# Optimization experiments

Measured on AMD Instinct MI355X. Metric: run time of the kernel, lower is better.

The kernel has to match this reference:

```python
import jax, jax.numpy as jnp
import numpy as np

B, SEQ, NVAR, DM, K = 2, 512, 64, 128, 2
SCALE = DM ** -0.5  # ScaledDotProductAttention scale, lsa=False so constant


def _period_branch(x4, Wel, bel, Wq, bq, Wk, bk, Wv, bv, Wo, bo, period):
    # x4: [B, DM(time), NVAR, DM(dim)] -- output of start_embed
    pad = (-DM) % period
    pn = (DM + pad) // period  # period_num
    xp = jnp.pad(x4, ((0, 0), (0, pad), (0, 0), (0, 0)))
    # torch .unfold(dim=1, size=period, step=period) -> [B, pn, NVAR, DM, period]
    xw = xp.reshape(B, pn, period, NVAR, DM).transpose(0, 1, 3, 4, 2)
    # emb_linear over the d_model (dim) axis
    xw = jnp.einsum('bqndl,ed->bqnel', xw, Wel) + bel[None, None, None, :, None]
    # -> [B, NVAR, dim, pn, period] then flatten to conv1d layout [bn, dim, L]
    X = xw.transpose(0, 2, 3, 1, 4).reshape(B * NVAR, DM, pn * period)
    # 1x1 Conv1d QKV projections over the channel (dim) axis
    q = jnp.einsum('bdl,ed->bel', X, Wq) + bq[None, :, None]
    k = jnp.einsum('bdl,ed->bel', X, Wk) + bk[None, :, None]
    v = jnp.einsum('bdl,ed->bel', X, Wv) + bv[None, :, None]
    q_s = q.reshape(B * NVAR, DM, pn, period).transpose(0, 1, 3, 2)  # [bn,dim,pl,pn]
    k_s = k.reshape(B * NVAR, DM, pn, period)                         # [bn,dim,pn,pl]
    v_s = v.reshape(B * NVAR, DM, pn, period).transpose(0, 1, 3, 2)  # [bn,dim,pl,pn]
    attn = jax.nn.softmax(jnp.einsum('bdip,bdpj->bdij', q_s, k_s) * SCALE, axis=-1)
    o = jnp.einsum('bdij,bdjp->bdip', attn, v_s)  # [bn, dim, period, pn]
    o = o.reshape(B * NVAR, DM, period * pn)[:, :, :DM]  # truncate to n_heads=DM
    return o @ Wo.T + bo  # to_out Linear(n_heads, n_heads), dropout eval-mode


def reference(x, W_emb, b_emb, W_start, b_start, Wel, bel, Wq, bq, Wk, bk, Wv, bv, Wo, bo, f1, f2):
    # inverted embedding: Linear(seq_len->d_model) over time, then permute -> [B, DM, NVAR]
    xe = (jnp.einsum('bsn,sd->bnd', x, W_emb) + b_emb).transpose(0, 2, 1)
    # FFT_for_Period amplitudes; top-k frequency indices f1,f2 are static (host-side in torch)
    amp = jnp.abs(jnp.fft.rfft(xe, axis=1)).mean(-1)  # [B, DM//2+1]
    pw = jax.nn.softmax(jnp.stack([amp[:, f1], amp[:, f2]], -1), axis=-1)  # [B, K]
    # start_embed: Linear(1 -> d_model) -> [B, DM, NVAR, DM]
    x4 = xe[..., None] * W_start + b_start
    outs = [_period_branch(x4, Wel, bel, Wq, bq, Wk, bk, Wv, bv, Wo, bo, DM // f)
            for f in (f1, f2)]
    res = jnp.stack(outs, -1)                      # [B*NVAR, DM, DM, K]
    pw_b = jnp.repeat(pw, NVAR, axis=0)            # [B*NVAR, K] (b-major order matches reshape)
    out = (res * pw_b[:, None, None, :]).sum(-1)
    return out.reshape(B, NVAR, DM, DM)


def setup_inputs() -> dict:
    key = jax.random.key(0)
    ks = jax.random.split(key, 16)
    s = 0.02
    d = {
        'x': jax.random.normal(ks[0], (B, SEQ, NVAR), jnp.float32),
        'W_emb': jax.random.normal(ks[1], (SEQ, DM), jnp.float32) * s,
        'b_emb': jax.random.normal(ks[2], (DM,), jnp.float32) * s,
        'W_start': jax.random.normal(ks[3], (DM,), jnp.float32) * s,
        'b_start': jax.random.normal(ks[4], (DM,), jnp.float32) * s,
        'Wel': jax.random.normal(ks[5], (DM, DM), jnp.float32) * s,
        'bel': jax.random.normal(ks[6], (DM,), jnp.float32) * s,
        'Wq': jax.random.normal(ks[7], (DM, DM), jnp.float32) * s,
        'bq': jax.random.normal(ks[8], (DM,), jnp.float32) * s,
        'Wk': jax.random.normal(ks[9], (DM, DM), jnp.float32) * s,
        'bk': jax.random.normal(ks[10], (DM,), jnp.float32) * s,
        'Wv': jax.random.normal(ks[11], (DM, DM), jnp.float32) * s,
        'bv': jax.random.normal(ks[12], (DM,), jnp.float32) * s,
        'Wo': jax.random.normal(ks[13], (DM, DM), jnp.float32) * s,
        'bo': jax.random.normal(ks[14], (DM,), jnp.float32) * s,
    }
    # host-side FFT period detection, mirroring torch's .detach().cpu().numpy() topk
    xe = np.einsum('bsn,sd->bnd', np.asarray(d['x']), np.asarray(d['W_emb'])) + np.asarray(d['b_emb'])
    xe = xe.transpose(0, 2, 1)  # [B, DM, NVAR]
    fl = np.abs(np.fft.rfft(xe, axis=1)).mean(0).mean(-1)
    fl[0] = 0.0
    top = np.argsort(-fl, kind='stable')[:K]
    d['f1'] = int(top[0])
    d['f2'] = int(top[1])
    return d
```

## Files before the change

kernel.cpp:

```cpp
#include <hip/hip_runtime.h>

#define DMD 128
#define NV 64
#define BB 2
#define SQ 512
#define NBN 128
#define ASCALE 0.08838834764831845f
#define L2E 1.4426950408889634f
#define CSC (ASCALE * L2E)

#define WS_XE  0
#define WS_PW  (WS_XE + NBN*DMD)
#define WS_VEC (WS_PW + 4)
#define WS_OB  (WS_VEC + 9*DMD)

__global__ __launch_bounds__(512) void k_xe(const float* __restrict__ x,
                                            const float* __restrict__ W_emb,
                                            const float* __restrict__ b_emb,
                                            float* __restrict__ ws) {
    int bn = blockIdx.x;
    int b = bn >> 6, n = bn & 63;
    int tid = threadIdx.x;
    int t = tid & 127, sc = tid >> 7;
    __shared__ float xsh[SQ];
    __shared__ float part[3][DMD];
    xsh[tid] = x[(b * SQ + tid) * NV + n];
    __syncthreads();
    float acc = 0.f;
    const float* W = W_emb + (sc * 128) * DMD + t;
#pragma unroll 8
    for (int s = 0; s < 128; ++s) acc = fmaf(xsh[sc * 128 + s], W[s * DMD], acc);
    if (sc) part[sc - 1][t] = acc;
    __syncthreads();
    if (sc == 0)
        ws[WS_XE + bn * DMD + t] = acc + part[0][t] + part[1][t] + part[2][t] + b_emb[t];
}

__global__ __launch_bounds__(128) void k_prep(const int* __restrict__ f1p,
                                              const int* __restrict__ f2p,
                                              const float* __restrict__ Wel, const float* __restrict__ bel,
                                              const float* __restrict__ W_start, const float* __restrict__ b_start,
                                              const float* __restrict__ Wq, const float* __restrict__ bq,
                                              const float* __restrict__ Wk, const float* __restrict__ bk,
                                              const float* __restrict__ Wv, const float* __restrict__ bv,
                                              float* __restrict__ ws) {
    int tid = threadIdx.x;
    __shared__ float ct[DMD], st[DMD];
    __shared__ float a2[2];
    __shared__ float A[DMD], C[DMD], BL[DMD];
    if (blockIdx.x < 2) {
        int b = blockIdx.x;
        float ang = (float)tid * 0.04908738521234052f;
        ct[tid] = cosf(ang);
        st[tid] = sinf(ang);
        __syncthreads();
        int k = tid >> 6;
        int n = tid & 63;
        int f = k ? f2p[0] : f1p[0];
        const float* xr = ws + WS_XE + (b * NV + n) * DMD;
        float re = 0.f, im = 0.f;
#pragma unroll 8
        for (int t = 0; t < DMD; ++t) {
            int ph = (f * t) & (DMD - 1);
            float v = xr[t];
            re = fmaf(v, ct[ph], re);
            im = fmaf(v, st[ph], im);
        }
        float amp = sqrtf(re * re + im * im);
        for (int off = 32; off > 0; off >>= 1) amp += __shfl_down(amp, off);
        if (n == 0) a2[k] = amp * (1.0f / NV);
        __syncthreads();
        if (tid == 0) {
            float m = fmaxf(a2[0], a2[1]);
            float e0 = expf(a2[0] - m), e1 = expf(a2[1] - m);
            float inv = 1.0f / (e0 + e1);
            ws[WS_PW + b * 2 + 0] = e0 * inv;
            ws[WS_PW + b * 2 + 1] = e1 * inv;
        }
    } else {
        int e = tid;
        float a = 0.f, c = 0.f;
        for (int d = 0; d < DMD; ++d) {
            float w = Wel[e * DMD + d];
            a = fmaf(w, W_start[d], a);
            c = fmaf(w, b_start[d], c);
        }
        A[e] = a;
        C[e] = c + bel[e];
        BL[e] = bel[e];
        __syncthreads();
        float aq = 0, cq = 0, pq = 0, ak = 0, ck = 0, pk = 0, av = 0, cv = 0, pv = 0;
        for (int d = 0; d < DMD; ++d) {
            float Ad = A[d], Cd = C[d], Bd = BL[d];
            float wq = Wq[e * DMD + d], wk = Wk[e * DMD + d], wv = Wv[e * DMD + d];
            aq = fmaf(wq, Ad, aq); cq = fmaf(wq, Cd, cq); pq = fmaf(wq, Bd, pq);
            ak = fmaf(wk, Ad, ak); ck = fmaf(wk, Cd, ck); pk = fmaf(wk, Bd, pk);
            av = fmaf(wv, Ad, av); cv = fmaf(wv, Cd, cv); pv = fmaf(wv, Bd, pv);
        }
        float* V = ws + WS_VEC;
        V[0 * DMD + e] = aq; V[1 * DMD + e] = cq + bq[e]; V[2 * DMD + e] = pq + bq[e];
        V[3 * DMD + e] = ak; V[4 * DMD + e] = ck + bk[e]; V[5 * DMD + e] = pk + bk[e];
        V[6 * DMD + e] = av; V[7 * DMD + e] = cv + bv[e]; V[8 * DMD + e] = pv + bv[e];
    }
}


__device__ __forceinline__ void attn_rank1(float pwv, const float (*Vsh)[4],
                                           const float* xs, float* __restrict__ ob,
                                           int rowbase, int tid) {
    float xi = xs[tid];
    float t[4], l[4], ax[4];
#pragma unroll
    for (int k = 0; k < 4; ++k) {
        float Aq = Vsh[0][k], Cq = Vsh[1][k], Ak = Vsh[3][k];
        t[k] = CSC * fmaf(xi, Aq, Cq) * Ak;
        l[k] = 0.f; ax[k] = 0.f;
    }
#pragma unroll 4
    for (int j = 0; j < DMD; ++j) {
        float xj = xs[j];
#pragma unroll
        for (int k = 0; k < 4; ++k) {
            float ev = exp2f(t[k] * xj);
            l[k] += ev;
            ax[k] = fmaf(ev, xj, ax[k]);
        }
    }
#pragma unroll
    for (int k = 0; k < 4; ++k) {
        float Av = Vsh[6][k], Cv = Vsh[7][k];
        float o = fmaf(Av, ax[k] / l[k], Cv);
        ob[rowbase + k * DMD + tid] = pwv * o;
    }
}

template<int PP, int NP, int EB>
__device__ __forceinline__ void attn_pow2(float pwv, const float (*Vsh)[4],
                                          const float* xs, float* __restrict__ ob,
                                          int rowbase, int tid) {
    const int UH = PP / 4;
    int lane4 = tid & 3, i0 = tid >> 2, jb = lane4 * UH;

    float xq[NP][UH], U2[UH];
#pragma unroll
    for (int u = 0; u < UH; ++u) {
        int j = jb + u;
        float s = 0.f;
#pragma unroll
        for (int q = 0; q < NP; ++q) { float xv = xs[q * PP + j]; xq[q][u] = xv; s += xv; }
        U2[u] = s;
    }
    const int NREP = (PP == 64) ? 2 : 1;
#pragma unroll
    for (int rep = 0; rep < NREP; ++rep) {
        int i = i0 + rep * 32;
        float G2[UH];
#pragma unroll
        for (int u = 0; u < UH; ++u) G2[u] = 0.f;
#pragma unroll
        for (int q = 0; q < NP; ++q) {
            float xi = xs[q * PP + i];
#pragma unroll
            for (int u = 0; u < UH; ++u) G2[u] = fmaf(xi, xq[q][u], G2[u]);
        }
#pragma unroll
        for (int eg = 0; eg < 4; eg += EB) {
            float d1[EB], d2[EB], l[EB];
            float accq[NP][EB];
#pragma unroll
            for (int k = 0; k < EB; ++k) {
                float t = CSC * Vsh[3][eg + k];
                d1[k] = t * Vsh[0][eg + k];
                d2[k] = t * Vsh[1][eg + k];
                l[k] = 0.f;
#pragma unroll
                for (int q = 0; q < NP; ++q) accq[q][k] = 0.f;
            }
#pragma unroll
            for (int u = 0; u < UH; ++u) {
                float gg = G2[u], uu = U2[u];
                float ev[EB];
#pragma unroll
                for (int k = 0; k < EB; ++k) ev[k] = exp2f(fmaf(d1[k], gg, d2[k] * uu));
#pragma unroll
                for (int k = 0; k < EB; ++k) {
                    l[k] += ev[k];
#pragma unroll
                    for (int q = 0; q < NP; ++q) accq[q][k] = fmaf(ev[k], xq[q][u], accq[q][k]);
                }
            }
#pragma unroll
            for (int k = 0; k < EB; ++k) { l[k] += __shfl_xor(l[k], 1); l[k] += __shfl_xor(l[k], 2); }
#pragma unroll
            for (int q = 0; q < NP; ++q)
#pragma unroll
                for (int k = 0; k < EB; ++k) {
                    accq[q][k] += __shfl_xor(accq[q][k], 1);
                    accq[q][k] += __shfl_xor(accq[q][k], 2);
                }
            if (lane4 == 0) {
#pragma unroll
                for (int k = 0; k < EB; ++k) {
                    float li = 1.f / l[k];
                    float Av = Vsh[6][eg + k], Cv = Vsh[7][eg + k];
#pragma unroll
                    for (int q = 0; q < NP; ++q) {
                        float o = fmaf(Av, accq[q][k] * li, Cv);
                        ob[rowbase + (eg + k) * DMD + i * NP + q] = pwv * o;
                    }
                }
            }
        }
    }
}

template<int UB>
__device__ __forceinline__ void attn_small(
    int P, int pn, int r, int Prows, float pwv,
    const float (*Vsh)[4], const float* xs, const float* U, const float* xt,
    float* W, float* __restrict__ ob, int rowbase, int tid)
{
    int GP = P + 1;
    int tot = Prows * P;
    unsigned mP = (4096u + (unsigned)P - 1u) / (unsigned)P;
    unsigned mpn = (4096u + (unsigned)pn - 1u) / (unsigned)pn;

    bool v0 = (tid < tot);
    int i0 = (int)(((unsigned)tid * mP) >> 12);
    int j0 = tid - i0 * P;
    bool A0 = (i0 < r), c0 = (j0 < r);
    float xtj0 = xt[j0], Uj0 = U[j0];
    float xti0 = A0 ? xt[i0] : 0.f;
    float g0 = 0.f;
    for (int p = 0; p < pn - 1; ++p) g0 = fmaf(xs[p * P + i0], xs[p * P + j0], g0);
    float Gx0 = (A0 && c0) ? fmaf(xti0, xtj0, g0) : g0;
    float Ux0 = (A0 && c0) ? Uj0 + xtj0 : Uj0;
    float Xw0 = (!A0 && c0) ? xtj0 : 0.f;
    float mw0 = c0 ? 1.f : 0.f;
    int wa0 = i0 * GP + j0;

    int idx1 = tid + 128;
    bool v1 = (idx1 < tot);
    int idx1c = v1 ? idx1 : 0;
    int i1 = (int)(((unsigned)idx1c * mP) >> 12);
    int j1 = idx1c - i1 * P;
    bool A1 = (i1 < r), c1 = (j1 < r);
    float xtj1 = xt[j1], Uj1 = U[j1];
    float xti1 = A1 ? xt[i1] : 0.f;
    float g1 = 0.f;
    for (int p = 0; p < pn - 1; ++p) g1 = fmaf(xs[p * P + i1], xs[p * P + j1], g1);
    float Gx1 = (A1 && c1) ? fmaf(xti1, xtj1, g1) : g1;
    float Ux1 = (A1 && c1) ? Uj1 + xtj1 : Uj1;
    float Xw1 = (!A1 && c1) ? xtj1 : 0.f;
    float mw1 = c1 ? 1.f : 0.f;
    int wa1 = i1 * GP + j1;

    int i2 = (int)(((unsigned)tid * mpn) >> 12);
    int p2 = tid - i2 * pn;
    bool lastp = (p2 == pn - 1);
    int row2 = i2 * GP;
    float xsr[UB];
#pragma unroll
    for (int j = 0; j < UB; ++j) {
        int idx = p2 * P + j;
        xsr[j] = (j < P && idx < DMD) ? xs[idx] : 0.f;
    }

    float s[4][2];
#pragma unroll
    for (int ec = 0; ec < 4; ++ec) {
        float Aq = Vsh[0][ec], Cq = Vsh[1][ec], Pq = Vsh[2][ec];
        float Ak = Vsh[3][ec], Ck = Vsh[4][ec], Pk = Vsh[5][ec];
        float t = CSC * Ak;
        float d1 = t * Aq, d2 = t * Cq, d3 = t * Pq;
        float ckpk = CSC * (Ck - Pk);
        float aS0 = A0 ? fmaf(Aq, xti0, Cq) : Pq;
        s[ec][0] = fmaf(d1, Gx0, fmaf(d2, Ux0, fmaf(d3, Xw0, (ckpk * aS0) * mw0)));
        float aS1 = A1 ? fmaf(Aq, xti1, Cq) : Pq;
        s[ec][1] = fmaf(d1, Gx1, fmaf(d2, Ux1, fmaf(d3, Xw1, (ckpk * aS1) * mw1)));
    }
#pragma unroll
    for (int ec = 0; ec < 4; ++ec) { s[ec][0] = exp2f(s[ec][0]); s[ec][1] = exp2f(s[ec][1]); }
#pragma unroll
    for (int ec = 0; ec < 4; ++ec) {
        if (v0) W[ec * 288 + wa0] = s[ec][0];
        if (v1) W[ec * 288 + wa1] = s[ec][1];
    }
    __syncthreads();

#pragma unroll
    for (int ec = 0; ec < 4; ++ec) {
        float Av = Vsh[6][ec], Cv = Vsh[7][ec], Pv = Vsh[8][ec];
        float l = 0.f, wr = 0.f, ax = 0.f;
#pragma unroll
        for (int j = 0; j < UB; ++j) {
            float w = W[ec * 288 + row2 + ((j < P) ? j : 0)];
            w = (j < P) ? w : 0.f;
            l += w;
            wr += (j < r) ? w : 0.f;
            ax = fmaf(w, xsr[j], ax);
        }
        float li = 1.f / l;
        float o;
        if (lastp) { float sl = wr * li; o = fmaf(Av, ax * li, fmaf(Cv, sl, Pv * (1.f - sl))); }
        else       o = fmaf(Av, ax * li, Cv);
        ob[rowbase + ec * DMD + tid] = pwv * o;
    }
}

template<int UH, int NP>
__device__ __forceinline__ void attn_midA(
    int P, int pn, int r, int Prows, float pwv,
    const float (*Vsh)[4], const float* xs, const float* U,
    const float* xt, float* __restrict__ ob, int rowbase, int tid)
{
    int lane4 = tid & 3;
    int i0 = tid >> 2;
    int jb = lane4 * UH;

    float Ur[UH], xtr[UH], xq0[UH], xq1[UH];
#pragma unroll
    for (int u = 0; u < UH; ++u) {
        int j = jb + u, jc = (j < P) ? j : 0;
        Ur[u] = U[jc];
        xtr[u] = xt[jc];
        xq0[u] = (j < DMD) ? xs[j] : 0.f;
        int i1x = P + j;
        xq1[u] = (i1x < DMD) ? xs[i1x] : 0.f;
    }
    int nrep = (Prows > 32) ? 2 : 1;
    for (int rep = 0; rep < nrep; ++rep) {
        int i = i0 + rep * 32;
        bool rowact = (i < Prows);
        int ic = rowact ? i : 0;
        float xtic = xt[ic];
        bool rowvalid = (ic < r);
        float g[UH];
#pragma unroll
        for (int u = 0; u < UH; ++u) g[u] = 0.f;
        for (int p = 0; p < pn - 1; ++p) {
            float xi = xs[p * P + ic];
#pragma unroll
            for (int u = 0; u < UH; ++u) {
                int j = jb + u, jc = (j < P) ? j : 0;
                g[u] = fmaf(xi, xs[p * P + jc], g[u]);
            }
        }
        for (int ec = 0; ec < 4; ++ec) {
            float Aq = Vsh[0][ec], Cq = Vsh[1][ec], Pq = Vsh[2][ec];
            float Ak = Vsh[3][ec], Ck = Vsh[4][ec], Pk = Vsh[5][ec];
            float Av = Vsh[6][ec], Cv = Vsh[7][ec], Pv = Vsh[8][ec];
            float c1 = CSC * Aq * Ak, c3 = CSC * Cq * Ak;
            float asi = CSC * (rowvalid ? fmaf(xtic, Aq, Cq) : Pq);

            float l0 = 0.f, l1 = 0.f, w0 = 0.f, w1 = 0.f;
            float accq[NP];
#pragma unroll
            for (int q = 0; q < NP; ++q) accq[q] = 0.f;
#pragma unroll
            for (int u = 0; u < UH; ++u) {
                int j = jb + u;
                float bK = (j < r) ? fmaf(xtr[u], Ak, Ck) : Pk;
                float S = fmaf(asi, bK, fmaf(c3, Ur[u], c1 * g[u]));
                float ev = exp2f(S);
                ev = (j < P) ? ev : 0.f;
                if (u & 1) l1 += ev; else l0 += ev;
                float evr = (j < r) ? ev : 0.f;
                if (u & 1) w1 += evr; else w0 += evr;
                accq[0] = fmaf(ev, xq0[u], accq[0]);
                if (NP >= 2) accq[1] = fmaf(ev, xq1[u], accq[1]);
#pragma unroll
                for (int q = 2; q < NP; ++q) {
                    int idx = q * P + j;
                    float xv = (idx < DMD) ? xs[idx] : 0.f;
                    accq[q] = fmaf(ev, xv, accq[q]);
                }
            }
            float l = l0 + l1, wr = w0 + w1;
            l += __shfl_xor(l, 1);  l += __shfl_xor(l, 2);
            wr += __shfl_xor(wr, 1); wr += __shfl_xor(wr, 2);
#pragma unroll
            for (int q = 0; q < NP; ++q) {
                if (q < pn) {
                    accq[q] += __shfl_xor(accq[q], 1);
                    accq[q] += __shfl_xor(accq[q], 2);
                }
            }
            if (lane4 == 0 && rowact) {
                float li = 1.f / l;
#pragma unroll
                for (int q = 0; q < NP; ++q) {
                    if (q < pn) {
                        int mo = i * pn + q;
                        if (mo < DMD) {
                            float o;
                            if (q == pn - 1) {
                                float sl = wr * li;
                                o = fmaf(Av, accq[q] * li, fmaf(Cv, sl, Pv * (1.f - sl)));
                            } else {
                                o = fmaf(Av, accq[q] * li, Cv);
                            }
                            ob[rowbase + ec * DMD + mo] = pwv * o;
                        }
                    }
                }
            }
        }
    }
}

__global__ __launch_bounds__(128) void k_attn(const int* __restrict__ f1p,
                                              const int* __restrict__ f2p,
                                              float* __restrict__ ws,
                                              float* __restrict__ outb) {
    int bn = blockIdx.y, b = bn >> 6;
    int e0 = blockIdx.x * 4;
    int br = blockIdx.z;
    int tid = threadIdx.x;

    __shared__ float xs[DMD], U[64], xt[64];
    __shared__ float Vsh[9][4];
    __shared__ float W[4 * 288];

    xs[tid] = ws[WS_XE + bn * DMD + tid];
    if (tid < 36) Vsh[tid >> 2][tid & 3] = ws[WS_VEC + (tid >> 2) * DMD + e0 + (tid & 3)];
    int f = br ? f2p[0] : f1p[0];
    float pwv = ws[WS_PW + b * 2 + br];
    float* ob = br ? outb : (ws + WS_OB);
    int rowbase = (bn * DMD + e0) * DMD;
    __syncthreads();

    int P = DMD / f;
    int pn = (DMD + P - 1) / P;
    int r = DMD - (pn - 1) * P;
    int Prows = (DMD + pn - 1) / pn;

    if (P == DMD) {
        attn_rank1(pwv, Vsh, xs, ob, rowbase, tid);
        return;
    }
    if (tid < P) {
        float s = 0.f;
        for (int p = 0; p < pn - 1; ++p) s += xs[p * P + tid];
        U[tid] = s;
        xt[tid] = (tid < r) ? xs[(pn - 1) * P + tid] : 0.f;
    }
    __syncthreads();

    if (P <= 4)       attn_small<4>(P, pn, r, Prows, pwv, Vsh, xs, U, xt, W, ob, rowbase, tid);
    else if (P <= 8)  attn_small<8>(P, pn, r, Prows, pwv, Vsh, xs, U, xt, W, ob, rowbase, tid);
    else if (P <= 16) attn_small<16>(P, pn, r, Prows, pwv, Vsh, xs, U, xt, W, ob, rowbase, tid);
    else if (P == 64) attn_pow2<64, 2, 2>(pwv, Vsh, xs, ob, rowbase, tid);
    else if (P == 32) attn_pow2<32, 4, 4>(pwv, Vsh, xs, ob, rowbase, tid);
    else if (P > 32)  attn_midA<16, 4>(P, pn, r, Prows, pwv, Vsh, xs, U, xt, ob, rowbase, tid);
    else              attn_midA<8, 8>(P, pn, r, Prows, pwv, Vsh, xs, U, xt, ob, rowbase, tid);
}

__global__ __launch_bounds__(256) void k_out(const float* __restrict__ Wo,
                                             const float* __restrict__ bo,
                                             const float* __restrict__ ws,
                                             float* __restrict__ out) {
    int blk = blockIdx.x;
    int bn0 = (blk >> 2) * 2;
    int e0  = (blk & 3) * 32;
    int tid = threadIdx.x;
    __shared__ __align__(16) float WTc[32 * 132];
    __shared__ __align__(16) float oT[2][32][36];
    int hg = tid & 31, eg = tid >> 5, h0 = hg * 4;

    float acc[2][4][4];
#pragma unroll
    for (int a = 0; a < 2; ++a)
#pragma unroll
        for (int c = 0; c < 4; ++c)
#pragma unroll
            for (int d = 0; d < 4; ++d) acc[a][c][d] = 0.f;

    for (int mc = 0; mc < 4; ++mc) {
        int m0 = mc * 32;
        __syncthreads();
        for (int idx = tid; idx < 4096; idx += 256) {
            int h = idx >> 5, mm = idx & 31;
            WTc[mm * 132 + h] = Wo[h * DMD + m0 + mm];
        }
        for (int idx = tid; idx < 2048; idx += 256) {
            int bnl = idx >> 10, rem = idx & 1023, e = rem >> 5, mm = rem & 31;
            int gi = ((bn0 + bnl) * DMD + e0 + e) * DMD + m0 + mm;
            oT[bnl][mm][e] = ws[WS_OB + gi] + out[gi];
        }
        __syncthreads();
#pragma unroll 4
        for (int mm = 0; mm < 32; ++mm) {
            const float4 wv = *reinterpret_cast<const float4*>(&WTc[mm * 132 + h0]);
            const float4 q0 = *reinterpret_cast<const float4*>(&oT[0][mm][eg * 4]);
            const float4 q1 = *reinterpret_cast<const float4*>(&oT[1][mm][eg * 4]);
            float ae[2][4] = {{q0.x, q0.y, q0.z, q0.w}, {q1.x, q1.y, q1.z, q1.w}};
#pragma unroll
            for (int bnl = 0; bnl < 2; ++bnl) {
#pragma unroll
                for (int el = 0; el < 4; ++el) {
                    float a = ae[bnl][el];
                    acc[bnl][el][0] = fmaf(a, wv.x, acc[bnl][el][0]);
                    acc[bnl][el][1] = fmaf(a, wv.y, acc[bnl][el][1]);
                    acc[bnl][el][2] = fmaf(a, wv.z, acc[bnl][el][2]);
                    acc[bnl][el][3] = fmaf(a, wv.w, acc[bnl][el][3]);
                }
            }
        }
    }
    const float4 bov = *reinterpret_cast<const float4*>(&bo[h0]);
#pragma unroll
    for (int bnl = 0; bnl < 2; ++bnl) {
#pragma unroll
        for (int el = 0; el < 4; ++el) {
            float4 res = { acc[bnl][el][0] + bov.x, acc[bnl][el][1] + bov.y,
                           acc[bnl][el][2] + bov.z, acc[bnl][el][3] + bov.w };
            int e = e0 + eg * 4 + el;
            *reinterpret_cast<float4*>(&out[((bn0 + bnl) * DMD + e) * DMD + h0]) = res;
        }
    }
}

extern "C" void kernel_launch(void* const* d_in, const int* in_sizes, int n_in,
                              void* d_out, int out_size, void* d_ws, size_t ws_size,
                              hipStream_t stream) {
    const float* x       = (const float*)d_in[0];
    const float* W_emb   = (const float*)d_in[1];
    const float* b_emb   = (const float*)d_in[2];
    const float* W_start = (const float*)d_in[3];
    const float* b_start = (const float*)d_in[4];
    const float* Wel     = (const float*)d_in[5];
    const float* bel     = (const float*)d_in[6];
    const float* Wq      = (const float*)d_in[7];
    const float* bq      = (const float*)d_in[8];
    const float* Wk      = (const float*)d_in[9];
    const float* bk      = (const float*)d_in[10];
    const float* Wv      = (const float*)d_in[11];
    const float* bv      = (const float*)d_in[12];
    const float* Wo      = (const float*)d_in[13];
    const float* bo      = (const float*)d_in[14];
    const int*   f1p     = (const int*)d_in[15];
    const int*   f2p     = (const int*)d_in[16];
    float* ws  = (float*)d_ws;
    float* out = (float*)d_out;

    k_xe<<<NBN, 512, 0, stream>>>(x, W_emb, b_emb, ws);
    k_prep<<<3, 128, 0, stream>>>(f1p, f2p, Wel, bel, W_start, b_start,
                                  Wq, bq, Wk, bk, Wv, bv, ws);
    k_attn<<<dim3(32, NBN, 2), 128, 0, stream>>>(f1p, f2p, ws, out);
    k_out<<<256, 256, 0, stream>>>(Wo, bo, ws, out);
}
```

Measured before the change: 86.28 us.

## Process four variables per k_xe block, eight channels per attention block, vectorize prep

k_xe now computes four variables per block from float4 loads of x, so each W_emb load is reused four times and the grid shrinks from 128 to 32 blocks. k_attn handles 8 output channels per block instead of 4, halving the grid and amortizing the shared xs, U and G setup. k_prep reads its weights as float4. The aim is fewer redundant loads and less per-block overhead, at the cost of fewer blocks (less parallelism) and more registers per thread.

```diff
diff --git a/kernel.cpp b/kernel.cpp
--- a/kernel.cpp
+++ b/kernel.cpp
@@ -18,22 +18,39 @@
                                             const float* __restrict__ W_emb,
                                             const float* __restrict__ b_emb,
                                             float* __restrict__ ws) {
-    int bn = blockIdx.x;
-    int b = bn >> 6, n = bn & 63;
+    int blk = blockIdx.x;
+    int b = blk >> 4, n0 = (blk & 15) * 4;
     int tid = threadIdx.x;
     int t = tid & 127, sc = tid >> 7;
-    __shared__ float xsh[SQ];
-    __shared__ float part[3][DMD];
-    xsh[tid] = x[(b * SQ + tid) * NV + n];
+    __shared__ __align__(16) float4 xsh[SQ];
+    __shared__ float part[3][DMD][4];
+    xsh[tid] = *reinterpret_cast<const float4*>(&x[(b * SQ + tid) * NV + n0]);
     __syncthreads();
-    float acc = 0.f;
+    float a0 = 0.f, a1 = 0.f, a2 = 0.f, a3 = 0.f;
     const float* W = W_emb + (sc * 128) * DMD + t;
 #pragma unroll 8
-    for (int s = 0; s < 128; ++s) acc = fmaf(xsh[sc * 128 + s], W[s * DMD], acc);
-    if (sc) part[sc - 1][t] = acc;
+    for (int s = 0; s < 128; ++s) {
+        float w = W[s * DMD];
+        float4 xv = xsh[sc * 128 + s];
+        a0 = fmaf(xv.x, w, a0); a1 = fmaf(xv.y, w, a1);
+        a2 = fmaf(xv.z, w, a2); a3 = fmaf(xv.w, w, a3);
+    }
+    if (sc) {
+        part[sc - 1][t][0] = a0; part[sc - 1][t][1] = a1;
+        part[sc - 1][t][2] = a2; part[sc - 1][t][3] = a3;
+    }
     __syncthreads();
-    if (sc == 0)
-        ws[WS_XE + bn * DMD + t] = acc + part[0][t] + part[1][t] + part[2][t] + b_emb[t];
+    if (sc == 0) {
+        float be = b_emb[t];
+        float r0 = a0 + part[0][t][0] + part[1][t][0] + part[2][t][0] + be;
+        float r1 = a1 + part[0][t][1] + part[1][t][1] + part[2][t][1] + be;
+        float r2 = a2 + part[0][t][2] + part[1][t][2] + part[2][t][2] + be;
+        float r3 = a3 + part[0][t][3] + part[1][t][3] + part[2][t][3] + be;
+        ws[WS_XE + (b * NV + n0 + 0) * DMD + t] = r0;
+        ws[WS_XE + (b * NV + n0 + 1) * DMD + t] = r1;
+        ws[WS_XE + (b * NV + n0 + 2) * DMD + t] = r2;
+        ws[WS_XE + (b * NV + n0 + 3) * DMD + t] = r3;
+    }
 }
 
 __global__ __launch_bounds__(128) void k_prep(const int* __restrict__ f1p,
@@ -47,7 +64,7 @@
     int tid = threadIdx.x;
     __shared__ float ct[DMD], st[DMD];
     __shared__ float a2[2];
-    __shared__ float A[DMD], C[DMD], BL[DMD];
+    __shared__ __align__(16) float A[DMD], C[DMD], BL[DMD];
     if (blockIdx.x < 2) {
         int b = blockIdx.x;
         float ang = (float)tid * 0.04908738521234052f;
@@ -80,22 +97,39 @@
     } else {
         int e = tid;
         float a = 0.f, c = 0.f;
-        for (int d = 0; d < DMD; ++d) {
-            float w = Wel[e * DMD + d];
-            a = fmaf(w, W_start[d], a);
-            c = fmaf(w, b_start[d], c);
+        const float4* We4 = reinterpret_cast<const float4*>(Wel + e * DMD);
+        const float4* Ws4 = reinterpret_cast<const float4*>(W_start);
+        const float4* Bs4 = reinterpret_cast<const float4*>(b_start);
+#pragma unroll 8
+        for (int d4 = 0; d4 < 32; ++d4) {
+            float4 w = We4[d4], s4 = Ws4[d4], t4 = Bs4[d4];
+            a = fmaf(w.x, s4.x, fmaf(w.y, s4.y, fmaf(w.z, s4.z, fmaf(w.w, s4.w, a))));
+            c = fmaf(w.x, t4.x, fmaf(w.y, t4.y, fmaf(w.z, t4.z, fmaf(w.w, t4.w, c))));
         }
         A[e] = a;
         C[e] = c + bel[e];
         BL[e] = bel[e];
         __syncthreads();
         float aq = 0, cq = 0, pq = 0, ak = 0, ck = 0, pk = 0, av = 0, cv = 0, pv = 0;
-        for (int d = 0; d < DMD; ++d) {
-            float Ad = A[d], Cd = C[d], Bd = BL[d];
-            float wq = Wq[e * DMD + d], wk = Wk[e * DMD + d], wv = Wv[e * DMD + d];
-            aq = fmaf(wq, Ad, aq); cq = fmaf(wq, Cd, cq); pq = fmaf(wq, Bd, pq);
-            ak = fmaf(wk, Ad, ak); ck = fmaf(wk, Cd, ck); pk = fmaf(wk, Bd, pk);
-            av = fmaf(wv, Ad, av); cv = fmaf(wv, Cd, cv); pv = fmaf(wv, Bd, pv);
+        const float4* Wq4 = reinterpret_cast<const float4*>(Wq + e * DMD);
+        const float4* Wk4 = reinterpret_cast<const float4*>(Wk + e * DMD);
+        const float4* Wv4 = reinterpret_cast<const float4*>(Wv + e * DMD);
+        const float4* A4 = reinterpret_cast<const float4*>(A);
+        const float4* C4 = reinterpret_cast<const float4*>(C);
+        const float4* B4 = reinterpret_cast<const float4*>(BL);
+#pragma unroll 4
+        for (int d4 = 0; d4 < 32; ++d4) {
+            float4 Ad = A4[d4], Cd = C4[d4], Bd = B4[d4];
+            float4 wq = Wq4[d4], wk = Wk4[d4], wv = Wv4[d4];
+            aq = fmaf(wq.x, Ad.x, fmaf(wq.y, Ad.y, fmaf(wq.z, Ad.z, fmaf(wq.w, Ad.w, aq))));
+            cq = fmaf(wq.x, Cd.x, fmaf(wq.y, Cd.y, fmaf(wq.z, Cd.z, fmaf(wq.w, Cd.w, cq))));
+            pq = fmaf(wq.x, Bd.x, fmaf(wq.y, Bd.y, fmaf(wq.z, Bd.z, fmaf(wq.w, Bd.w, pq))));
+            ak = fmaf(wk.x, Ad.x, fmaf(wk.y, Ad.y, fmaf(wk.z, Ad.z, fmaf(wk.w, Ad.w, ak))));
+            ck = fmaf(wk.x, Cd.x, fmaf(wk.y, Cd.y, fmaf(wk.z, Cd.z, fmaf(wk.w, Cd.w, ck))));
+            pk = fmaf(wk.x, Bd.x, fmaf(wk.y, Bd.y, fmaf(wk.z, Bd.z, fmaf(wk.w, Bd.w, pk))));
+            av = fmaf(wv.x, Ad.x, fmaf(wv.y, Ad.y, fmaf(wv.z, Ad.z, fmaf(wv.w, Ad.w, av))));
+            cv = fmaf(wv.x, Cd.x, fmaf(wv.y, Cd.y, fmaf(wv.z, Cd.z, fmaf(wv.w, Cd.w, cv))));
+            pv = fmaf(wv.x, Bd.x, fmaf(wv.y, Bd.y, fmaf(wv.z, Bd.z, fmaf(wv.w, Bd.w, pv))));
         }
         float* V = ws + WS_VEC;
         V[0 * DMD + e] = aq; V[1 * DMD + e] = cq + bq[e]; V[2 * DMD + e] = pq + bq[e];
@@ -105,37 +139,35 @@
 }
 
 
-__device__ __forceinline__ void attn_rank1(float pwv, const float (*Vsh)[4],
+__device__ __forceinline__ void attn_rank1(float pwv, const float (*Vsh)[8],
                                            const float* xs, float* __restrict__ ob,
                                            int rowbase, int tid) {
     float xi = xs[tid];
-    float t[4], l[4], ax[4];
-#pragma unroll
-    for (int k = 0; k < 4; ++k) {
-        float Aq = Vsh[0][k], Cq = Vsh[1][k], Ak = Vsh[3][k];
-        t[k] = CSC * fmaf(xi, Aq, Cq) * Ak;
+    float t[8], l[8], ax[8];
+#pragma unroll
+    for (int k = 0; k < 8; ++k) {
+        t[k] = CSC * fmaf(xi, Vsh[0][k], Vsh[1][k]) * Vsh[3][k];
         l[k] = 0.f; ax[k] = 0.f;
     }
 #pragma unroll 4
     for (int j = 0; j < DMD; ++j) {
         float xj = xs[j];
 #pragma unroll
-        for (int k = 0; k < 4; ++k) {
+        for (int k = 0; k < 8; ++k) {
             float ev = exp2f(t[k] * xj);
             l[k] += ev;
             ax[k] = fmaf(ev, xj, ax[k]);
         }
     }
 #pragma unroll
-    for (int k = 0; k < 4; ++k) {
-        float Av = Vsh[6][k], Cv = Vsh[7][k];
-        float o = fmaf(Av, ax[k] / l[k], Cv);
+    for (int k = 0; k < 8; ++k) {
+        float o = fmaf(Vsh[6][k], ax[k] / l[k], Vsh[7][k]);
         ob[rowbase + k * DMD + tid] = pwv * o;
     }
 }
 
 template<int PP, int NP, int EB>
-__device__ __forceinline__ void attn_pow2(float pwv, const float (*Vsh)[4],
+__device__ __forceinline__ void attn_pow2(float pwv, const float (*Vsh)[8],
                                           const float* xs, float* __restrict__ ob,
                                           int rowbase, int tid) {
     const int UH = PP / 4;
@@ -164,7 +196,7 @@
             for (int u = 0; u < UH; ++u) G2[u] = fmaf(xi, xq[q][u], G2[u]);
         }
 #pragma unroll
-        for (int eg = 0; eg < 4; eg += EB) {
+        for (int eg = 0; eg < 8; eg += EB) {
             float d1[EB], d2[EB], l[EB];
             float accq[NP][EB];
 #pragma unroll
@@ -217,7 +249,7 @@
 template<int UB>
 __device__ __forceinline__ void attn_small(
     int P, int pn, int r, int Prows, float pwv,
-    const float (*Vsh)[4], const float* xs, const float* U, const float* xt,
+    const float (*Vsh)[8], const float* xs, const float* U, const float* xt,
     float* W, float* __restrict__ ob, int rowbase, int tid)
 {
     int GP = P + 1;
@@ -266,30 +298,30 @@
         xsr[j] = (j < P && idx < DMD) ? xs[idx] : 0.f;
     }
 
-    float s[4][2];
-#pragma unroll
-    for (int ec = 0; ec < 4; ++ec) {
+    float sv[8][2];
+#pragma unroll
+    for (int ec = 0; ec < 8; ++ec) {
         float Aq = Vsh[0][ec], Cq = Vsh[1][ec], Pq = Vsh[2][ec];
         float Ak = Vsh[3][ec], Ck = Vsh[4][ec], Pk = Vsh[5][ec];
         float t = CSC * Ak;
         float d1 = t * Aq, d2 = t * Cq, d3 = t * Pq;
         float ckpk = CSC * (Ck - Pk);
         float aS0 = A0 ? fmaf(Aq, xti0, Cq) : Pq;
-        s[ec][0] = fmaf(d1, Gx0, fmaf(d2, Ux0, fmaf(d3, Xw0, (ckpk * aS0) * mw0)));
+        sv[ec][0] = fmaf(d1, Gx0, fmaf(d2, Ux0, fmaf(d3, Xw0, (ckpk * aS0) * mw0)));
         float aS1 = A1 ? fmaf(Aq, xti1, Cq) : Pq;
-        s[ec][1] = fmaf(d1, Gx1, fmaf(d2, Ux1, fmaf(d3, Xw1, (ckpk * aS1) * mw1)));
-    }
-#pragma unroll
-    for (int ec = 0; ec < 4; ++ec) { s[ec][0] = exp2f(s[ec][0]); s[ec][1] = exp2f(s[ec][1]); }
-#pragma unroll
-    for (int ec = 0; ec < 4; ++ec) {
-        if (v0) W[ec * 288 + wa0] = s[ec][0];
-        if (v1) W[ec * 288 + wa1] = s[ec][1];
+        sv[ec][1] = fmaf(d1, Gx1, fmaf(d2, Ux1, fmaf(d3, Xw1, (ckpk * aS1) * mw1)));
+    }
+#pragma unroll
+    for (int ec = 0; ec < 8; ++ec) { sv[ec][0] = exp2f(sv[ec][0]); sv[ec][1] = exp2f(sv[ec][1]); }
+#pragma unroll
+    for (int ec = 0; ec < 8; ++ec) {
+        if (v0) W[ec * 288 + wa0] = sv[ec][0];
+        if (v1) W[ec * 288 + wa1] = sv[ec][1];
     }
     __syncthreads();
 
 #pragma unroll
-    for (int ec = 0; ec < 4; ++ec) {
+    for (int ec = 0; ec < 8; ++ec) {
         float Av = Vsh[6][ec], Cv = Vsh[7][ec], Pv = Vsh[8][ec];
         float l = 0.f, wr = 0.f, ax = 0.f;
 #pragma unroll
@@ -311,7 +343,7 @@
 template<int UH, int NP>
 __device__ __forceinline__ void attn_midA(
     int P, int pn, int r, int Prows, float pwv,
-    const float (*Vsh)[4], const float* xs, const float* U,
+    const float (*Vsh)[8], const float* xs, const float* U,
     const float* xt, float* __restrict__ ob, int rowbase, int tid)
 {
     int lane4 = tid & 3;
@@ -346,7 +378,7 @@
                 g[u] = fmaf(xi, xs[p * P + jc], g[u]);
             }
         }
-        for (int ec = 0; ec < 4; ++ec) {
+        for (int ec = 0; ec < 8; ++ec) {
             float Aq = Vsh[0][ec], Cq = Vsh[1][ec], Pq = Vsh[2][ec];
             float Ak = Vsh[3][ec], Ck = Vsh[4][ec], Pk = Vsh[5][ec];
             float Av = Vsh[6][ec], Cv = Vsh[7][ec], Pv = Vsh[8][ec];
@@ -414,16 +446,16 @@
                                               float* __restrict__ ws,
                                               float* __restrict__ outb) {
     int bn = blockIdx.y, b = bn >> 6;
-    int e0 = blockIdx.x * 4;
+    int e0 = blockIdx.x * 8;
     int br = blockIdx.z;
     int tid = threadIdx.x;
 
     __shared__ float xs[DMD], U[64], xt[64];
-    __shared__ float Vsh[9][4];
-    __shared__ float W[4 * 288];
+    __shared__ float Vsh[9][8];
+    __shared__ float W[8 * 288];
 
     xs[tid] = ws[WS_XE + bn * DMD + tid];
-    if (tid < 36) Vsh[tid >> 2][tid & 3] = ws[WS_VEC + (tid >> 2) * DMD + e0 + (tid & 3)];
+    if (tid < 72) Vsh[tid >> 3][tid & 7] = ws[WS_VEC + (tid >> 3) * DMD + e0 + (tid & 7)];
     int f = br ? f2p[0] : f1p[0];
     float pwv = ws[WS_PW + b * 2 + br];
     float* ob = br ? outb : (ws + WS_OB);
@@ -450,7 +482,7 @@
     if (P <= 4)       attn_small<4>(P, pn, r, Prows, pwv, Vsh, xs, U, xt, W, ob, rowbase, tid);
     else if (P <= 8)  attn_small<8>(P, pn, r, Prows, pwv, Vsh, xs, U, xt, W, ob, rowbase, tid);
     else if (P <= 16) attn_small<16>(P, pn, r, Prows, pwv, Vsh, xs, U, xt, W, ob, rowbase, tid);
-    else if (P == 64) attn_pow2<64, 2, 2>(pwv, Vsh, xs, ob, rowbase, tid);
+    else if (P == 64) attn_pow2<64, 2, 4>(pwv, Vsh, xs, ob, rowbase, tid);
     else if (P == 32) attn_pow2<32, 4, 4>(pwv, Vsh, xs, ob, rowbase, tid);
     else if (P > 32)  attn_midA<16, 4>(P, pn, r, Prows, pwv, Vsh, xs, U, xt, ob, rowbase, tid);
     else              attn_midA<8, 8>(P, pn, r, Prows, pwv, Vsh, xs, U, xt, ob, rowbase, tid);
@@ -544,9 +576,9 @@
     float* ws  = (float*)d_ws;
     float* out = (float*)d_out;
 
-    k_xe<<<NBN, 512, 0, stream>>>(x, W_emb, b_emb, ws);
+    k_xe<<<32, 512, 0, stream>>>(x, W_emb, b_emb, ws);
     k_prep<<<3, 128, 0, stream>>>(f1p, f2p, Wel, bel, W_start, b_start,
                                   Wq, bq, Wk, bk, Wv, bv, ws);
-    k_attn<<<dim3(32, NBN, 2), 128, 0, stream>>>(f1p, f2p, ws, out);
+    k_attn<<<dim3(16, NBN, 2), 128, 0, stream>>>(f1p, f2p, ws, out);
     k_out<<<256, 256, 0, stream>>>(Wo, bo, ws, out);
 }
```

After: 94.06 us. 1.09x slower.
